# Performance work log

Measured on AMD Instinct MI355X. Metric: run time of the kernel, lower is better.

The kernel has to match this reference:

```python
import jax, jax.numpy as jnp
import numpy as np

N, E, B, ROWS, IN, HID, JKO, FEAT, OH, OUT = 200000, 6400000, 64, 128, 128, 6, 4, 2560, 20, 2

def _leaky(x, s):
    return jnp.where(x >= 0, x, s * x)

def _ln(x, g, b, eps=1e-5):
    mu = jnp.mean(x, -1, keepdims=True)
    v = jnp.mean((x - mu) ** 2, -1, keepdims=True)
    return (x - mu) * jax.lax.rsqrt(v + eps) * g + b

def setup_inputs():
    key = jax.random.key(0)
    ks = jax.random.split(key, 32)
    def w(k, shape, fan_in):
        return jax.random.normal(k, shape, jnp.float32) * (1.0 / np.sqrt(fan_in))
    inp = {
        'x': jax.random.normal(ks[0], (N, IN), jnp.float32),
        'edge_index': jax.random.randint(ks[1], (2, E), 0, N, jnp.int32),
        'batch': jnp.sort(jax.random.randint(ks[2], (N,), 0, B, jnp.int32)),
        'features': jax.random.normal(ks[3], (B, ROWS, FEAT), jnp.float32),
        'one_hot': jax.random.uniform(ks[4], (B, OH), jnp.float32),
        # GATv2Conv params (heads=1)
        'W_l': w(ks[5], (IN, HID), IN), 'b_l': jnp.zeros((HID,)),
        'W_r': w(ks[6], (IN, HID), IN), 'b_r': jnp.zeros((HID,)),
        'att': w(ks[7], (HID,), HID), 'conv_b': jnp.zeros((HID,)),
        # BasicGNN final lin after JK (6 -> 4)
        'jk_W': w(ks[8], (HID, JKO), HID), 'jk_b': jnp.zeros((JKO,)),
        # MLP chain on features
        'l1_W': w(ks[9], (FEAT, 256), FEAT), 'l1_b': jnp.zeros((256,)),
        'ln1_g': jnp.ones((256,)), 'ln1_b': jnp.zeros((256,)),
        'l2_W': w(ks[10], (256, 64), 256), 'l2_b': jnp.zeros((64,)),
        'ln2_g': jnp.ones((64,)), 'ln2_b': jnp.zeros((64,)),
        'l3_W': w(ks[11], (64, 8), 64), 'l3_b': jnp.zeros((8,)),
        'ln3_g': jnp.ones((8,)), 'ln3_b': jnp.zeros((8,)),
        # flattening: rows*8 -> 32
        'fl_W': w(ks[12], (ROWS * 8, 32), ROWS * 8), 'fl_b': jnp.zeros((32,)),
        'ln4_g': jnp.ones((32,)), 'ln4_b': jnp.zeros((32,)),
        # output: 4 + 32 + 20 = 56 -> OUT
        'out_W': w(ks[13], (56, OUT), 56), 'out_b': jnp.zeros((OUT,)),
    }
    return inp

def _forward(x, features, one_hot, W_l, b_l, W_r, b_r, att, conv_b, jk_W, jk_b,
             l1_W, l1_b, ln1_g, ln1_b, l2_W, l2_b, ln2_g, ln2_b, l3_W, l3_b, ln3_g, ln3_b,
             fl_W, fl_b, ln4_g, ln4_b, out_W, out_b, edge_index, batch):
    n = x.shape[0]
    # GATv2Conv, heads=1: separate source/target transforms
    xl = x @ W_l + b_l  # [N,6] source/message features
    xr = x @ W_r + b_r  # [N,6] target features
    loops = jnp.arange(n, dtype=edge_index.dtype)
    src = jnp.concatenate([edge_index[0], loops])  # add self loops
    dst = jnp.concatenate([edge_index[1], loops])
    e = _leaky(xl[src] + xr[dst], 0.2)             # [E+N,6]
    score = e @ att                                 # [E+N]
    m = jax.lax.stop_gradient(jax.ops.segment_max(score, dst, num_segments=n))
    p = jnp.exp(score - m[dst])
    z = jax.ops.segment_sum(p, dst, num_segments=n)
    alpha = p / z[dst]                              # segment softmax over incoming edges
    agg = jax.ops.segment_sum(alpha[:, None] * xl[src], dst, num_segments=n) + conv_b
    x1 = _leaky(agg, 0.01)                          # BasicGNN act ('leakyrelu')
    # JK-LSTM with a single layer collapses to identity (softmax over 1 element)
    h = x1 @ jk_W + jk_b                            # [N,4]
    # global mean pool per graph
    nb = features.shape[0]
    sums = jax.ops.segment_sum(h, batch, num_segments=nb)
    cnt = jax.ops.segment_sum(jnp.ones((n,), h.dtype), batch, num_segments=nb)
    xgcn = sums / jnp.maximum(cnt, 1.0)[:, None]    # [B,4]
    # MLP on features (dropout = identity in eval)
    f = _leaky(_ln(features @ l1_W + l1_b, ln1_g, ln1_b), 0.01)
    f = _leaky(_ln(f @ l2_W + l2_b, ln2_g, ln2_b), 0.01)
    f = _leaky(_ln(f @ l3_W + l3_b, ln3_g, ln3_b), 0.01)  # [B,ROWS,8]
    flat = f.reshape(nb, -1)
    xf = _leaky(_ln(flat @ fl_W + fl_b, ln4_g, ln4_b), 0.01)  # [B,32]
    cat = jnp.concatenate([xgcn, xf, one_hot], axis=1)        # [B,56]
    return cat @ out_W + out_b

def reference(x, features, one_hot, W_l, b_l, W_r, b_r, att, conv_b, jk_W, jk_b,
              l1_W, l1_b, ln1_g, ln1_b, l2_W, l2_b, ln2_g, ln2_b, l3_W, l3_b, ln3_g, ln3_b,
              fl_W, fl_b, ln4_g, ln4_b, out_W, out_b, edge_index, batch):
    return _forward(x, features, one_hot, W_l, b_l, W_r, b_r, att, conv_b, jk_W, jk_b,
                    l1_W, l1_b, ln1_g, ln1_b, l2_W, l2_b, ln2_g, ln2_b, l3_W, l3_b, ln3_g, ln3_b,
                    fl_W, fl_b, ln4_g, ln4_b, out_W, out_b, edge_index, batch)
```

## Files before the change

kernel.cpp:

```cpp
#include <hip/hip_runtime.h>
#include <cstdint>
#include <cstddef>

#define N_NODES 200000
#define N_EDGES 6400000
#define NB      64
#define MROWS   8192
#define FEAT    2560

#define BSZ   256
#define NBK   782
#define EBLK  512
#define ETILE 12500
#define BCAP  8960
#define NXB   768
#define GEMMB 256
#define MLPRB 512

typedef __attribute__((ext_vector_type(8))) short bf16x8;
typedef __attribute__((ext_vector_type(4))) float f32x4;

__device__ __forceinline__ unsigned short bf16rne(float f) {
    unsigned u = __builtin_bit_cast(unsigned, f);
    u += 0x7fffu + ((u >> 16) & 1u);
    return (unsigned short)(u >> 16);
}

__device__ __forceinline__ float bf16f(unsigned short h) {
    return __builtin_bit_cast(float, (unsigned)h << 16);
}

__device__ __forceinline__ void async_cp16(const void* g, void* l) {
    __builtin_amdgcn_global_load_lds(
        (const __attribute__((address_space(1))) unsigned int*)g,
        (__attribute__((address_space(3))) unsigned int*)l, 16, 0, 0);
}

__device__ __forceinline__ void edge_acc(
    uint4 g, const float* xrd, const float* attv, float& z, float* agg)
{
    float xls[6];
    xls[0] = __builtin_bit_cast(float, g.x << 16);
    xls[1] = __builtin_bit_cast(float, g.x & 0xffff0000u);
    xls[2] = __builtin_bit_cast(float, g.y << 16);
    xls[3] = __builtin_bit_cast(float, g.y & 0xffff0000u);
    xls[4] = __builtin_bit_cast(float, g.z << 16);
    xls[5] = __builtin_bit_cast(float, g.z & 0xffff0000u);
    float sc = 0.f;
#pragma unroll
    for (int j = 0; j < 6; j++) {
        float e = xls[j] + xrd[j];
        e = (e >= 0.f) ? e : 0.2f * e;
        sc += attv[j] * e;
    }
    const float p = __expf(sc);
    z += p;
#pragma unroll
    for (int j = 0; j < 6; j++) agg[j] += p * xls[j];
}


__device__ __forceinline__ void nx_body(
    const int nxi, const int nstride,
    const float* __restrict__ x,
    const float* __restrict__ Wl, const float* __restrict__ bl,
    const float* __restrict__ Wr, const float* __restrict__ br,
    unsigned short* __restrict__ xlb, float* __restrict__ xr)
{
    const int t = threadIdx.x;
    const int l = t & 15;

    float wl[48], wr[48];
#pragma unroll
    for (int q = 0; q < 12; q++) {
        *(float4*)&wl[q * 4] = *(const float4*)(Wl + 48 * l + 4 * q);
        *(float4*)&wr[q * 4] = *(const float4*)(Wr + 48 * l + 4 * q);
    }
    for (int g = nxi; g < N_NODES / 16; g += nstride) {
        const int node = g * 16 + (t >> 4);
        float xv[8];
        *(float4*)&xv[0] = *(const float4*)(x + (size_t)node * 128 + l * 8);
        *(float4*)&xv[4] = *(const float4*)(x + (size_t)node * 128 + l * 8 + 4);

        float al[6] = {}, ar[6] = {};
#pragma unroll
        for (int i = 0; i < 8; i++) {
#pragma unroll
            for (int j = 0; j < 6; j++) {
                al[j] += xv[i] * wl[i * 6 + j];
                ar[j] += xv[i] * wr[i * 6 + j];
            }
        }
#pragma unroll
        for (int off = 8; off >= 1; off >>= 1) {
#pragma unroll
            for (int j = 0; j < 6; j++) {
                al[j] += __shfl_xor(al[j], off);
                ar[j] += __shfl_xor(ar[j], off);
            }
        }
        if (l == 0) {
            union { unsigned short h[8]; uint4 v; } u;
#pragma unroll
            for (int j = 0; j < 6; j++) u.h[j] = bf16rne(al[j] + bl[j]);
            u.h[6] = 0; u.h[7] = 0;
            *(uint4*)(xlb + (size_t)node * 8) = u.v;
            float4 r0; float2 r1;
            r0.x = ar[0] + br[0]; r0.y = ar[1] + br[1];
            r0.z = ar[2] + br[2]; r0.w = ar[3] + br[3];
            r1.x = ar[4] + br[4]; r1.y = ar[5] + br[5];
            *(float4*)(xr + (size_t)node * 8) = r0;
            *(float2*)(xr + (size_t)node * 8 + 4) = r1;
        }
    }
}

__device__ __forceinline__ void eb_body(
    const int bid, char* smem,
    const int* __restrict__ ei, int* __restrict__ cursor, int* __restrict__ pairs)
{
    int* sorted = (int*)smem;
    int* hb     = sorted + ETILE;
    int* cur    = hb + NBK + 1;
    int* gbl    = cur + NBK;
    int* wsum   = gbl + NBK;
    const int t = threadIdx.x;
    const int lane = t & 63, wid = t >> 6;
    const int base = bid * ETILE;

    for (int b = t; b < NBK; b += 256) cur[b] = 0;
    __syncthreads();

    for (int i = t; i < ETILE; i += 256)
        atomicAdd(&cur[ei[N_EDGES + base + i] >> 8], 1);
    __syncthreads();

    int c[4]; int lsum = 0;
#pragma unroll
    for (int q = 0; q < 4; q++) {
        const int b = 4 * t + q;
        c[q] = (b < NBK) ? cur[b] : 0;
        lsum += c[q];
    }
    int v = lsum;
#pragma unroll
    for (int d = 1; d < 64; d <<= 1) {
        const int o = __shfl_up(v, d);
        if (lane >= d) v += o;
    }
    if (lane == 63) wsum[wid] = v;
    __syncthreads();
    int off = 0;
#pragma unroll
    for (int w = 0; w < 3; w++) if (w < wid) off += wsum[w];
    int run = off + v - lsum;

    int mygb[4];
#pragma unroll
    for (int q = 0; q < 4; q++) {
        const int b = 4 * t + q;
        mygb[q] = (b < NBK && c[q] > 0) ? atomicAdd(&cursor[b], c[q]) : 0;
    }

#pragma unroll
    for (int q = 0; q < 4; q++) {
        const int b = 4 * t + q;
        if (b <= NBK) hb[b] = run;
        if (b < NBK) cur[b] = run;
        run += c[q];
    }
    __syncthreads();

    for (int i = t; i < ETILE; i += 256) {
        const int d = ei[N_EDGES + base + i];
        const int s = ei[base + i];
        const int pos = atomicAdd(&cur[d >> 8], 1);
        sorted[pos] = (s << 8) | (d & 255);
    }
#pragma unroll
    for (int q = 0; q < 4; q++) {
        const int b = 4 * t + q;
        if (b < NBK) gbl[b] = mygb[q];
    }
    __syncthreads();

    const int grp = t >> 4, gl = t & 15;
    for (int b = grp; b < NBK; b += 16) {
        const int st = hb[b];
        const int cnt = hb[b + 1] - st;
        int* dst = pairs + b * BCAP + gbl[b];
        for (int i = gl; i < cnt; i += 16)
            dst[i] = sorted[st + i];
    }
}

__device__ __forceinline__ void gemm_l1_body(
    const int bx, const int by, char* smem,
    const float* __restrict__ A, const unsigned short* __restrict__ Bt,
    const float* __restrict__ bias, float* __restrict__ C)
{
    unsigned short (*As)[64 * 64] = (unsigned short(*)[64 * 64])smem;
    unsigned short (*Bs)[128 * 64] =
        (unsigned short(*)[128 * 64])(smem + 2 * 64 * 64 * sizeof(short));
    const int K = FEAT, N = 256;
    const int t = threadIdx.x;
    const int w = t >> 6, l = t & 63;
    const int l15 = l & 15, quad = l >> 4;
    const int wm = (w & 1) * 32, wn = (w >> 1) * 64;
    const int gm0 = bx * 64;
    const int gn0 = by * 128;
    const int r8 = l >> 3;
    const int c8 = (l & 7) ^ r8;
    const int ar = t >> 2;
    const int ac0 = (t & 3) * 2;

    f32x4 acc[2][4];
#pragma unroll
    for (int mt = 0; mt < 2; mt++)
#pragma unroll
        for (int nt = 0; nt < 4; nt++) acc[mt][nt] = (f32x4){0.f, 0.f, 0.f, 0.f};

    const int niter = K / 64;

#pragma unroll
    for (int c = 0; c < 4; c++) {
        const int j = w * 4 + c;
        async_cp16(Bt + (size_t)(gn0 + j * 8 + r8) * K + c8 * 8, &Bs[0][j * 512]);
    }
    {
        const float* src = A + (size_t)(gm0 + ar) * K + ac0 * 8;
        float4 v0 = *(const float4*)src;
        float4 v1 = *(const float4*)(src + 4);
        float4 v2 = *(const float4*)(src + 8);
        float4 v3 = *(const float4*)(src + 12);
        union { unsigned short h[8]; uint4 u; } p0, p1;
        p0.h[0] = bf16rne(v0.x); p0.h[1] = bf16rne(v0.y);
        p0.h[2] = bf16rne(v0.z); p0.h[3] = bf16rne(v0.w);
        p0.h[4] = bf16rne(v1.x); p0.h[5] = bf16rne(v1.y);
        p0.h[6] = bf16rne(v1.z); p0.h[7] = bf16rne(v1.w);
        p1.h[0] = bf16rne(v2.x); p1.h[1] = bf16rne(v2.y);
        p1.h[2] = bf16rne(v2.z); p1.h[3] = bf16rne(v2.w);
        p1.h[4] = bf16rne(v3.x); p1.h[5] = bf16rne(v3.y);
        p1.h[6] = bf16rne(v3.z); p1.h[7] = bf16rne(v3.w);
        *(uint4*)&As[0][ar * 64 + ((ac0 + 0) ^ (ar & 7)) * 8] = p0.u;
        *(uint4*)&As[0][ar * 64 + ((ac0 + 1) ^ (ar & 7)) * 8] = p1.u;
    }

    int p = 0;
    for (int i = 0; i < niter; i++) {
        __syncthreads();
        const bool nxt = (i + 1 < niter);
        float4 v0, v1, v2, v3;
        if (nxt) {
            const int k1 = (i + 1) * 64;
#pragma unroll
            for (int c = 0; c < 4; c++) {
                const int j = w * 4 + c;
                async_cp16(Bt + (size_t)(gn0 + j * 8 + r8) * K + k1 + c8 * 8,
                           &Bs[p ^ 1][j * 512]);
            }
            const float* src = A + (size_t)(gm0 + ar) * K + k1 + ac0 * 8;
            v0 = *(const float4*)src;
            v1 = *(const float4*)(src + 4);
            v2 = *(const float4*)(src + 8);
            v3 = *(const float4*)(src + 12);
        }
#pragma unroll
        for (int kki = 0; kki < 2; kki++) {
            bf16x8 af[2], bfr[4];
#pragma unroll
            for (int mt = 0; mt < 2; mt++) {
                const int m = wm + mt * 16 + l15;
                af[mt] = *(const bf16x8*)&As[p][m * 64 + (((quad + 4 * kki) ^ (m & 7)) * 8)];
            }
#pragma unroll
            for (int nt = 0; nt < 4; nt++) {
                const int n = wn + nt * 16 + l15;
                bfr[nt] = *(const bf16x8*)&Bs[p][n * 64 + (((quad + 4 * kki) ^ (n & 7)) * 8)];
            }
#pragma unroll
            for (int mt = 0; mt < 2; mt++)
#pragma unroll
                for (int nt = 0; nt < 4; nt++)
                    acc[mt][nt] = __builtin_amdgcn_mfma_f32_16x16x32_bf16(
                        af[mt], bfr[nt], acc[mt][nt], 0, 0, 0);
        }
        if (nxt) {
            union { unsigned short h[8]; uint4 u; } p0, p1;
            p0.h[0] = bf16rne(v0.x); p0.h[1] = bf16rne(v0.y);
            p0.h[2] = bf16rne(v0.z); p0.h[3] = bf16rne(v0.w);
            p0.h[4] = bf16rne(v1.x); p0.h[5] = bf16rne(v1.y);
            p0.h[6] = bf16rne(v1.z); p0.h[7] = bf16rne(v1.w);
            p1.h[0] = bf16rne(v2.x); p1.h[1] = bf16rne(v2.y);
            p1.h[2] = bf16rne(v2.z); p1.h[3] = bf16rne(v2.w);
            p1.h[4] = bf16rne(v3.x); p1.h[5] = bf16rne(v3.y);
            p1.h[6] = bf16rne(v3.z); p1.h[7] = bf16rne(v3.w);
            *(uint4*)&As[p ^ 1][ar * 64 + ((ac0 + 0) ^ (ar & 7)) * 8] = p0.u;
            *(uint4*)&As[p ^ 1][ar * 64 + ((ac0 + 1) ^ (ar & 7)) * 8] = p1.u;
        }
        p ^= 1;
    }
#pragma unroll
    for (int nt = 0; nt < 4; nt++) {
        const int col = gn0 + wn + nt * 16 + l15;
        const float bv = bias[col];
#pragma unroll
        for (int mt = 0; mt < 2; mt++)
#pragma unroll
            for (int rr = 0; rr < 4; rr++) {
                const int row = gm0 + wm + mt * 16 + quad * 4 + rr;
                C[(size_t)row * N + col] = acc[mt][nt][rr] + bv;
            }
    }
}

__device__ __forceinline__ void br_body(
    const int bid, char* smem,
    const int* __restrict__ pairs, const int* __restrict__ cursor,
    const unsigned short* __restrict__ xlb, const float* __restrict__ xr,
    const float* __restrict__ att, const float* __restrict__ conv_b,
    const float* __restrict__ jkW, const float* __restrict__ jkb,
    const int* __restrict__ batch,
    float* __restrict__ gsum, float* __restrict__ gcnt)
{
    int* sorted = (int*)smem;
    int* hist   = sorted + BCAP;
    int* wtot   = hist + 256;
    const int t = threadIdx.x;
    const int lane = t & 63, wid = t >> 6;
    const int d0 = bid * BSZ + t;

    float xrd[6];
    if (d0 < N_NODES) {
        float4 a = *(const float4*)(xr + (size_t)d0 * 8);
        float2 b = *(const float2*)(xr + (size_t)d0 * 8 + 4);
        xrd[0] = a.x; xrd[1] = a.y; xrd[2] = a.z;
        xrd[3] = a.w; xrd[4] = b.x; xrd[5] = b.y;
    } else {
#pragma unroll
        for (int j = 0; j < 6; j++) xrd[j] = 0.f;
    }
    float attv[6];
#pragma unroll
    for (int j = 0; j < 6; j++) attv[j] = att[j];

    float z = 0.f, agg[6] = {};
    const uint4* xl4 = (const uint4*)xlb;
    const int e0 = bid * BCAP;
    const int e1 = e0 + cursor[bid];

    for (int c0 = e0; c0 < e1; c0 += BCAP) {
        const int rem = e1 - c0;
        const int cnt_chunk = (rem < BCAP) ? rem : BCAP;
        hist[t] = 0;
        __syncthreads();
        for (int i = t; i < cnt_chunk; i += 256)
            atomicAdd(&hist[pairs[c0 + i] & 255], 1);
        __syncthreads();
        const int h = hist[t];
        int v = h;
#pragma unroll
        for (int d = 1; d < 64; d <<= 1) {
            int o = __shfl_up(v, d);
            if (lane >= d) v += o;
        }
        if (lane == 63) wtot[wid] = v;
        __syncthreads();
        int off = 0;
#pragma unroll
        for (int wv = 0; wv < 3; wv++) if (wv < wid) off += wtot[wv];
        const int my_start = v - h + off;
        const int my_cnt = h;
        __syncthreads();
        hist[t] = my_start;
        __syncthreads();
        for (int i = t; i < cnt_chunk; i += 256) {
            const int pv = pairs[c0 + i];
            const int pos = atomicAdd(&hist[pv & 255], 1);
            sorted[pos] = ((unsigned)pv) >> 8;
        }
        __syncthreads();
        int i = 0;
        for (; i + 4 <= my_cnt; i += 4) {
            const int s0 = sorted[my_start + i];
            const int s1 = sorted[my_start + i + 1];
            const int s2 = sorted[my_start + i + 2];
            const int s3 = sorted[my_start + i + 3];
            const uint4 g0 = xl4[s0], g1 = xl4[s1], g2 = xl4[s2], g3 = xl4[s3];
            edge_acc(g0, xrd, attv, z, agg);
            edge_acc(g1, xrd, attv, z, agg);
            edge_acc(g2, xrd, attv, z, agg);
            edge_acc(g3, xrd, attv, z, agg);
        }
        for (; i < my_cnt; i++) {
            const uint4 g = xl4[sorted[my_start + i]];
            edge_acc(g, xrd, attv, z, agg);
        }
        __syncthreads();
    }

    float hh[4] = {0.f, 0.f, 0.f, 0.f};
    float cw = 0.f;
    int b = 0;
    if (d0 < N_NODES) {
        const uint4 g = xl4[d0];
        float xld[6];
        xld[0] = __builtin_bit_cast(float, g.x << 16);
        xld[1] = __builtin_bit_cast(float, g.x & 0xffff0000u);
        xld[2] = __builtin_bit_cast(float, g.y << 16);
        xld[3] = __builtin_bit_cast(float, g.y & 0xffff0000u);
        xld[4] = __builtin_bit_cast(float, g.z << 16);
        xld[5] = __builtin_bit_cast(float, g.z & 0xffff0000u);
        float sc = 0.f;
#pragma unroll
        for (int j = 0; j < 6; j++) {
            float e = xld[j] + xrd[j];
            e = (e >= 0.f) ? e : 0.2f * e;
            sc += attv[j] * e;
        }
        const float p = __expf(sc);
        const float zz = z + p;
#pragma unroll
        for (int c = 0; c < 4; c++) hh[c] = jkb[c];
#pragma unroll
        for (int j = 0; j < 6; j++) {
            float aj = (agg[j] + p * xld[j]) / zz + conv_b[j];
            aj = (aj >= 0.f) ? aj : 0.01f * aj;
#pragma unroll
            for (int c = 0; c < 4; c++) hh[c] += aj * jkW[j * 4 + c];
        }
        b = batch[d0];
        cw = 1.f;
    }
    const int b0 = __shfl(b, 0);
    if (__all(b == b0)) {
#pragma unroll
        for (int off2 = 32; off2 >= 1; off2 >>= 1) {
#pragma unroll
            for (int c = 0; c < 4; c++) hh[c] += __shfl_xor(hh[c], off2);
            cw += __shfl_xor(cw, off2);
        }
        if (lane == 0 && cw > 0.f) {
#pragma unroll
            for (int c = 0; c < 4; c++) atomicAdd(gsum + b0 * 4 + c, hh[c]);
            atomicAdd(gcnt + b0, cw);
        }
    } else if (cw > 0.f) {
#pragma unroll
        for (int c = 0; c < 4; c++) atomicAdd(gsum + b * 4 + c, hh[c]);
        atomicAdd(gcnt + b, cw);
    }
}

__device__ __forceinline__ void mlp_rows_body(
    const int bid, char* smem,
    const float* __restrict__ f1, const unsigned short* __restrict__ w2t,
    const float* __restrict__ ln1_g, const float* __restrict__ ln1_b,
    const float* __restrict__ l2_b,
    const float* __restrict__ ln2_g, const float* __restrict__ ln2_b,
    const float* __restrict__ l3_W, const float* __restrict__ l3_b,
    const float* __restrict__ ln3_g, const float* __restrict__ ln3_b,
    float* __restrict__ f3)
{
    unsigned short* W2 = (unsigned short*)smem;
    const int t = threadIdx.x;
    const int w = t >> 6, l = t & 63;

    for (int i = t; i < 16384; i += 256) {
        const int j = i >> 8, k = i & 255;
        W2[k * 66 + j] = w2t[i];
    }
    const float4 g1 = *(const float4*)(ln1_g + 4 * l);
    const float4 b1 = *(const float4*)(ln1_b + 4 * l);
    const float bo2 = l2_b[l], g2 = ln2_g[l], b2 = ln2_b[l];
    float w3r[8];
    *(float4*)&w3r[0] = *(const float4*)(l3_W + l * 8);
    *(float4*)&w3r[4] = *(const float4*)(l3_W + l * 8 + 4);
    float g3[8], b3[8], bo3[8];
#pragma unroll
    for (int c = 0; c < 8; c++) {
        g3[c] = ln3_g[c]; b3[c] = ln3_b[c]; bo3[c] = l3_b[c];
    }
    __syncthreads();

#pragma unroll 1
    for (int i4 = 0; i4 < 4; i4++) {
        const int row = bid * 16 + w * 4 + i4;
        const float4 v = *(const float4*)(f1 + (size_t)row * 256 + 4 * l);
        float s = v.x + v.y + v.z + v.w;
        float s2 = v.x * v.x + v.y * v.y + v.z * v.z + v.w * v.w;
#pragma unroll
        for (int o = 32; o >= 1; o >>= 1) {
            s += __shfl_xor(s, o);
            s2 += __shfl_xor(s2, o);
        }
        const float mu = s * (1.0f / 256.0f);
        const float rs = rsqrtf(s2 * (1.0f / 256.0f) - mu * mu + 1e-5f);
        float y[4];
        y[0] = (v.x - mu) * rs * g1.x + b1.x;
        y[1] = (v.y - mu) * rs * g1.y + b1.y;
        y[2] = (v.z - mu) * rs * g1.z + b1.z;
        y[3] = (v.w - mu) * rs * g1.w + b1.w;
#pragma unroll
        for (int i = 0; i < 4; i++) y[i] = (y[i] >= 0.f) ? y[i] : 0.01f * y[i];

        float acc = bo2;
#pragma unroll 4
        for (int k0 = 0; k0 < 64; k0++) {
            const float yv0 = __shfl(y[0], k0);
            const float yv1 = __shfl(y[1], k0);
            const float yv2 = __shfl(y[2], k0);
            const float yv3 = __shfl(y[3], k0);
            const int kb = k0 * 264 + l;
            acc += yv0 * bf16f(W2[kb]);
            acc += yv1 * bf16f(W2[kb + 66]);
            acc += yv2 * bf16f(W2[kb + 132]);
            acc += yv3 * bf16f(W2[kb + 198]);
        }
        float s1 = acc, q1 = acc * acc;
#pragma unroll
        for (int o = 32; o >= 1; o >>= 1) {
            s1 += __shfl_xor(s1, o);
            q1 += __shfl_xor(q1, o);
        }
        const float mu2 = s1 * (1.0f / 64.0f);
        const float rs2 = rsqrtf(q1 * (1.0f / 64.0f) - mu2 * mu2 + 1e-5f);
        float y2 = (acc - mu2) * rs2 * g2 + b2;
        y2 = (y2 >= 0.f) ? y2 : 0.01f * y2;

        float p8[8];
#pragma unroll
        for (int c = 0; c < 8; c++) p8[c] = y2 * w3r[c];
#pragma unroll
        for (int o = 32; o >= 1; o >>= 1)
#pragma unroll
            for (int c = 0; c < 8; c++) p8[c] += __shfl_xor(p8[c], o);
#pragma unroll
        for (int c = 0; c < 8; c++) p8[c] += bo3[c];
        float s3 = 0.f;
#pragma unroll
        for (int c = 0; c < 8; c++) s3 += p8[c];
        const float mu3 = s3 * 0.125f;
        float q3 = 0.f;
#pragma unroll
        for (int c = 0; c < 8; c++) { const float d = p8[c] - mu3; q3 += d * d; }
        const float rs3 = rsqrtf(q3 * 0.125f + 1e-5f);
        if (l == 0) {
            float o8[8];
#pragma unroll
            for (int c = 0; c < 8; c++) {
                float yy = (p8[c] - mu3) * rs3 * g3[c] + b3[c];
                o8[c] = (yy >= 0.f) ? yy : 0.01f * yy;
            }
            *(float4*)(f3 + (size_t)row * 8) = *(float4*)&o8[0];
            *(float4*)(f3 + (size_t)row * 8 + 4) = *(float4*)&o8[4];
        }
    }
}


__global__ __launch_bounds__(256) void node_xform(
    const float* __restrict__ x,
    const float* __restrict__ Wl, const float* __restrict__ bl,
    const float* __restrict__ Wr, const float* __restrict__ br,
    unsigned short* __restrict__ xlb, float* __restrict__ xr)
{
    nx_body(blockIdx.x, N_NODES / 16, x, Wl, bl, Wr, br, xlb, xr);
}

__global__ __launch_bounds__(256) void edge_bucket(
    const int* __restrict__ ei, int* __restrict__ cursor, int* __restrict__ pairs)
{
    __shared__ __align__(16) char smem[59408];
    eb_body(blockIdx.x, smem, ei, cursor, pairs);
}

__global__ __launch_bounds__(256) void mfma_gemm_l1(
    const float* __restrict__ A, const unsigned short* __restrict__ Bt,
    const float* __restrict__ bias, float* __restrict__ C)
{
    __shared__ __align__(16) char smem[49152];
    gemm_l1_body(blockIdx.x, blockIdx.y, smem, A, Bt, bias, C);
}

__global__ __launch_bounds__(256) void bucket_reduce(
    const int* __restrict__ pairs, const int* __restrict__ cursor,
    const unsigned short* __restrict__ xlb, const float* __restrict__ xr,
    const float* __restrict__ att, const float* __restrict__ conv_b,
    const float* __restrict__ jkW, const float* __restrict__ jkb,
    const int* __restrict__ batch,
    float* __restrict__ gsum, float* __restrict__ gcnt)
{
    __shared__ __align__(16) char smem[36880];
    br_body(blockIdx.x, smem, pairs, cursor, xlb, xr, att, conv_b, jkW, jkb,
            batch, gsum, gcnt);
}

__global__ __launch_bounds__(256) void fused_front(
    const float* __restrict__ x,
    const float* __restrict__ Wl, const float* __restrict__ bl,
    const float* __restrict__ Wr, const float* __restrict__ br,
    unsigned short* __restrict__ xlb, float* __restrict__ xr,
    const int* __restrict__ ei, int* __restrict__ cursor, int* __restrict__ pairs,
    const float* __restrict__ A, const unsigned short* __restrict__ Bt,
    const float* __restrict__ bias, float* __restrict__ C)
{
    __shared__ __align__(16) char smem[59408];
    const int bid = blockIdx.x;
    const int role = bid % 3;
    const int q = bid / 3;
    if (role == 0) {
        eb_body(q, smem, ei, cursor, pairs);
    } else if (role == 1 && q < GEMMB) {
        gemm_l1_body(q & 127, q >> 7, smem, A, Bt, bias, C);
    } else {
        const int nxi = (role == 2) ? q : EBLK + (q - GEMMB);
        nx_body(nxi, NXB, x, Wl, bl, Wr, br, xlb, xr);
    }
}

__global__ __launch_bounds__(256, 4) void fused_back(
    const int* __restrict__ pairs, const int* __restrict__ cursor,
    const unsigned short* __restrict__ xlb, const float* __restrict__ xr,
    const float* __restrict__ att, const float* __restrict__ conv_b,
    const float* __restrict__ jkW, const float* __restrict__ jkb,
    const int* __restrict__ batch,
    float* __restrict__ gsum, float* __restrict__ gcnt,
    const float* __restrict__ f1, const unsigned short* __restrict__ w2t,
    const float* __restrict__ ln1_g, const float* __restrict__ ln1_b,
    const float* __restrict__ l2_b,
    const float* __restrict__ ln2_g, const float* __restrict__ ln2_b,
    const float* __restrict__ l3_W, const float* __restrict__ l3_b,
    const float* __restrict__ ln3_g, const float* __restrict__ ln3_b,
    float* __restrict__ f3)
{
    __shared__ __align__(16) char smem[36880];
    const int bid = blockIdx.x;
    if (bid < NBK) {
        br_body(bid, smem, pairs, cursor, xlb, xr, att, conv_b, jkW, jkb,
                batch, gsum, gcnt);
    } else {
        mlp_rows_body(bid - NBK, smem, f1, w2t, ln1_g, ln1_b, l2_b,
                      ln2_g, ln2_b, l3_W, l3_b, ln3_g, ln3_b, f3);
    }
}

__global__ __launch_bounds__(256) void flat_final(
    const float* __restrict__ f3, const float* __restrict__ W,
    const float* __restrict__ bb,
    const float* __restrict__ g, const float* __restrict__ b,
    const float* __restrict__ gsum, const float* __restrict__ gcnt,
    const float* __restrict__ onehot,
    const float* __restrict__ Wo, const float* __restrict__ bo,
    float* __restrict__ out)
{
    __shared__ float sf[1024];
    __shared__ float sp[8][32];
    __shared__ float sxf[32];
    const int t = threadIdx.x;
    const int gb = blockIdx.x;
    *(float4*)&sf[t * 4] = *(const float4*)(f3 + (size_t)gb * 1024 + t * 4);
    __syncthreads();
    const int c = t & 31, part = t >> 5;
    float acc = 0.f;
    for (int k = part * 128; k < part * 128 + 128; k++) acc += sf[k] * W[k * 32 + c];
    sp[part][c] = acc;
    __syncthreads();
    if (t < 32) {
        float v = bb[t];
#pragma unroll
        for (int p = 0; p < 8; p++) v += sp[p][t];
        float s = v, s2 = v * v;
#pragma unroll
        for (int off = 16; off >= 1; off >>= 1) {
            s += __shfl_xor(s, off);
            s2 += __shfl_xor(s2, off);
        }
        const float mu = s * (1.0f / 32.0f);
        const float var = s2 * (1.0f / 32.0f) - mu * mu;
        float y = (v - mu) * rsqrtf(var + 1e-5f) * g[t] + b[t];
        sxf[t] = (y >= 0.f) ? y : 0.01f * y;
    }
    __syncthreads();
    if (t < 2) {
        const int o = t;
        float cnt = gcnt[gb];
        cnt = (cnt > 1.f) ? cnt : 1.f;
        float a2 = bo[o];
#pragma unroll
        for (int j = 0; j < 4; j++)  a2 += (gsum[gb * 4 + j] / cnt) * Wo[j * 2 + o];
#pragma unroll
        for (int j = 0; j < 32; j++) a2 += sxf[j] * Wo[(4 + j) * 2 + o];
#pragma unroll
        for (int j = 0; j < 20; j++) a2 += onehot[gb * 20 + j] * Wo[(36 + j) * 2 + o];
        out[gb * 2 + o] = a2;
    }
}

__global__ __launch_bounds__(256) void castT(
    const float* __restrict__ W, unsigned short* __restrict__ Wt, int K, int N)
{
    const int k = blockIdx.x * 256 + threadIdx.x;
    const int n = blockIdx.y;
    if (k < K) Wt[(size_t)n * K + k] = bf16rne(W[(size_t)k * N + n]);
}


__global__ __launch_bounds__(256) void mfma_gemm_l2(
    const unsigned short* __restrict__ Ab, const unsigned short* __restrict__ Bt,
    const float* __restrict__ bias, float* __restrict__ C,
    int M, int N, int K)
{
    __shared__ unsigned short As[32 * 64];
    __shared__ unsigned short Bs[64 * 64];
    const int t = threadIdx.x;
    const int w = t >> 6, l = t & 63;
    const int l15 = l & 15, quad = l >> 4;
    const int gm0 = blockIdx.x * 32;
    const int gn0 = blockIdx.y * 64;
    const int r8 = l >> 3;
    const int c8 = (l & 7) ^ r8;

    f32x4 acc[2];
    acc[0] = (f32x4){0.f, 0.f, 0.f, 0.f};
    acc[1] = (f32x4){0.f, 0.f, 0.f, 0.f};

    for (int k0 = 0; k0 < K; k0 += 64) {
#pragma unroll
        for (int c = 0; c < 2; c++) {
            const int j = w * 2 + c;
            async_cp16(Bt + (size_t)(gn0 + j * 8 + r8) * K + k0 + c8 * 8,
                       &Bs[j * 512]);
        }
        async_cp16(Ab + (size_t)(gm0 + w * 8 + r8) * K + k0 + c8 * 8, &As[w * 512]);
        __syncthreads();
#pragma unroll
        for (int kki = 0; kki < 2; kki++) {
            bf16x8 af[2], bfr;
#pragma unroll
            for (int mt = 0; mt < 2; mt++) {
                const int m = mt * 16 + l15;
                af[mt] = *(const bf16x8*)&As[m * 64 + (((quad + 4 * kki) ^ (m & 7)) * 8)];
            }
            const int n = w * 16 + l15;
            bfr = *(const bf16x8*)&Bs[n * 64 + (((quad + 4 * kki) ^ (n & 7)) * 8)];
#pragma unroll
            for (int mt = 0; mt < 2; mt++)
                acc[mt] = __builtin_amdgcn_mfma_f32_16x16x32_bf16(
                    af[mt], bfr, acc[mt], 0, 0, 0);
        }
        __syncthreads();
    }
    const int col = gn0 + w * 16 + l15;
    const float bv = bias[col];
#pragma unroll
    for (int mt = 0; mt < 2; mt++)
#pragma unroll
        for (int rr = 0; rr < 4; rr++) {
            const int row = gm0 + mt * 16 + quad * 4 + rr;
            C[(size_t)row * N + col] = acc[mt][rr] + bv;
        }
}

__global__ __launch_bounds__(256) void ln_leaky_c256(
    const float* __restrict__ f, unsigned short* __restrict__ out,
    const float* __restrict__ g, const float* __restrict__ b)
{
    const int row = blockIdx.x;
    const int t = threadIdx.x;
    float v = f[(size_t)row * 256 + t];
    float s = v, s2 = v * v;
#pragma unroll
    for (int off = 32; off >= 1; off >>= 1) {
        s += __shfl_xor(s, off);
        s2 += __shfl_xor(s2, off);
    }
    __shared__ float ws[4], ws2[4];
    const int wid = t >> 6, lane = t & 63;
    if (lane == 0) { ws[wid] = s; ws2[wid] = s2; }
    __syncthreads();
    const float S = ws[0] + ws[1] + ws[2] + ws[3];
    const float S2 = ws2[0] + ws2[1] + ws2[2] + ws2[3];
    const float mu = S * (1.0f / 256.0f);
    const float var = S2 * (1.0f / 256.0f) - mu * mu;
    float y = (v - mu) * rsqrtf(var + 1e-5f) * g[t] + b[t];
    y = (y >= 0.f) ? y : 0.01f * y;
    out[(size_t)row * 256 + t] = bf16rne(y);
}

__global__ __launch_bounds__(256) void ln_leaky_c64(
    float* __restrict__ f, const float* __restrict__ g, const float* __restrict__ b)
{
    const int wid = threadIdx.x >> 6, lane = threadIdx.x & 63;
    const int row = blockIdx.x * 4 + wid;
    float v = f[(size_t)row * 64 + lane];
    float s = v, s2 = v * v;
#pragma unroll
    for (int off = 32; off >= 1; off >>= 1) {
        s += __shfl_xor(s, off);
        s2 += __shfl_xor(s2, off);
    }
    const float mu = s * (1.0f / 64.0f);
    const float var = s2 * (1.0f / 64.0f) - mu * mu;
    float y = (v - mu) * rsqrtf(var + 1e-5f) * g[lane] + b[lane];
    f[(size_t)row * 64 + lane] = (y >= 0.f) ? y : 0.01f * y;
}

__global__ __launch_bounds__(256) void l3_ln_leaky(
    const float* __restrict__ f2, const float* __restrict__ W3,
    const float* __restrict__ b3,
    const float* __restrict__ g, const float* __restrict__ b,
    float* __restrict__ f3)
{
    __shared__ float sW[64 * 8];
    const int t = threadIdx.x;
    sW[t] = W3[t]; sW[t + 256] = W3[t + 256];
    __syncthreads();
    const int row = blockIdx.x * 32 + (t >> 3);
    const int c = t & 7;
    float acc = b3[c];
    const float* fr = f2 + (size_t)row * 64;
#pragma unroll 8
    for (int k = 0; k < 64; k++) acc += fr[k] * sW[k * 8 + c];
    float s = acc, s2 = acc * acc;
#pragma unroll
    for (int off = 4; off >= 1; off >>= 1) {
        s += __shfl_xor(s, off);
        s2 += __shfl_xor(s2, off);
    }
    const float mu = s * (1.0f / 8.0f);
    const float var = s2 * (1.0f / 8.0f) - mu * mu;
    float y = (acc - mu) * rsqrtf(var + 1e-5f) * g[c] + b[c];
    f3[(size_t)row * 8 + c] = (y >= 0.f) ? y : 0.01f * y;
}

__global__ __launch_bounds__(256) void flat_ln_leaky(
    const float* __restrict__ f3, const float* __restrict__ W,
    const float* __restrict__ bb,
    const float* __restrict__ g, const float* __restrict__ b,
    float* __restrict__ xf)
{
    __shared__ float sf[1024];
    __shared__ float sp[8][32];
    const int t = threadIdx.x;
    const int gb = blockIdx.x;
    *(float4*)&sf[t * 4] = *(const float4*)(f3 + (size_t)gb * 1024 + t * 4);
    __syncthreads();
    const int c = t & 31, part = t >> 5;
    float acc = 0.f;
    for (int k = part * 128; k < part * 128 + 128; k++) acc += sf[k] * W[k * 32 + c];
    sp[part][c] = acc;
    __syncthreads();
    if (t < 32) {
        float v = bb[t];
#pragma unroll
        for (int p = 0; p < 8; p++) v += sp[p][t];
        float s = v, s2 = v * v;
#pragma unroll
        for (int off = 16; off >= 1; off >>= 1) {
            s += __shfl_xor(s, off);
            s2 += __shfl_xor(s2, off);
        }
        const float mu = s * (1.0f / 32.0f);
        const float var = s2 * (1.0f / 32.0f) - mu * mu;
        float y = (v - mu) * rsqrtf(var + 1e-5f) * g[t] + b[t];
        xf[gb * 32 + t] = (y >= 0.f) ? y : 0.01f * y;
    }
}

__global__ __launch_bounds__(128) void final_out(
    const float* __restrict__ gsum, const float* __restrict__ gcnt,
    const float* __restrict__ xf, const float* __restrict__ onehot,
    const float* __restrict__ Wo, const float* __restrict__ bo,
    float* __restrict__ out)
{
    const int t = threadIdx.x;
    const int gb = t >> 1, o = t & 1;
    float cnt = gcnt[gb];
    cnt = (cnt > 1.f) ? cnt : 1.f;
    float acc = bo[o];
#pragma unroll
    for (int j = 0; j < 4; j++)  acc += (gsum[gb * 4 + j] / cnt) * Wo[j * 2 + o];
#pragma unroll
    for (int j = 0; j < 32; j++) acc += xf[gb * 32 + j] * Wo[(4 + j) * 2 + o];
#pragma unroll
    for (int j = 0; j < 20; j++) acc += onehot[gb * 20 + j] * Wo[(36 + j) * 2 + o];
    out[t] = acc;
}

extern "C" void kernel_launch(void* const* d_in, const int* in_sizes, int n_in,
                              void* d_out, int out_size, void* d_ws, size_t ws_size,
                              hipStream_t stream)
{
    const float* x        = (const float*)d_in[0];
    const int*   ei       = (const int*)d_in[1];
    const int*   batch    = (const int*)d_in[2];
    const float* features = (const float*)d_in[3];
    const float* one_hot  = (const float*)d_in[4];
    const float* W_l   = (const float*)d_in[5];
    const float* b_l   = (const float*)d_in[6];
    const float* W_r   = (const float*)d_in[7];
    const float* b_r   = (const float*)d_in[8];
    const float* att   = (const float*)d_in[9];
    const float* conv_b = (const float*)d_in[10];
    const float* jk_W  = (const float*)d_in[11];
    const float* jk_b  = (const float*)d_in[12];
    const float* l1_W  = (const float*)d_in[13];
    const float* l1_b  = (const float*)d_in[14];
    const float* ln1_g = (const float*)d_in[15];
    const float* ln1_b = (const float*)d_in[16];
    const float* l2_W  = (const float*)d_in[17];
    const float* l2_b  = (const float*)d_in[18];
    const float* ln2_g = (const float*)d_in[19];
    const float* ln2_b = (const float*)d_in[20];
    const float* l3_W  = (const float*)d_in[21];
    const float* l3_b  = (const float*)d_in[22];
    const float* ln3_g = (const float*)d_in[23];
    const float* ln3_b = (const float*)d_in[24];
    const float* fl_W  = (const float*)d_in[25];
    const float* fl_b  = (const float*)d_in[26];
    const float* ln4_g = (const float*)d_in[27];
    const float* ln4_b = (const float*)d_in[28];
    const float* out_W = (const float*)d_in[29];
    const float* out_b = (const float*)d_in[30];
    (void)in_sizes; (void)n_in; (void)out_size;

    float* ws = (float*)d_ws;
    unsigned short* xlb = (unsigned short*)(ws + 0);
    float* xr   = ws + 800000;
    unsigned short* w1t = (unsigned short*)(ws + 2400000);
    unsigned short* w2t = (unsigned short*)(ws + 2727680);
    float* gsum   = ws + 2735872;
    float* gcnt   = ws + 2736128;
    int*   cursor = (int*)(ws + 2736192);
    int* pairs = (int*)(ws + 2737024);

    const bool fuse = ws_size >= (size_t)13481344 * 4;

    hipMemsetAsync(gsum, 0, 1102 * sizeof(float), stream);

    castT<<<dim3(10, 256), 256, 0, stream>>>(l1_W, w1t, FEAT, 256);
    castT<<<dim3(1, 64), 256, 0, stream>>>(l2_W, w2t, 256, 64);

    if (fuse) {
        float* f1 = ws + 9743744;
        float* f3 = ws + 13413760;
        fused_front<<<EBLK + GEMMB + NXB, 256, 0, stream>>>(
            x, W_l, b_l, W_r, b_r, xlb, xr,
            ei, cursor, pairs,
            features, w1t, l1_b, f1);
        fused_back<<<NBK + MLPRB, 256, 0, stream>>>(
            pairs, cursor, xlb, xr, att, conv_b, jk_W, jk_b, batch,
            gsum, gcnt,
            f1, w2t, ln1_g, ln1_b, l2_b, ln2_g, ln2_b,
            l3_W, l3_b, ln3_g, ln3_b, f3);
        flat_final<<<NB, 256, 0, stream>>>(
            f3, fl_W, fl_b, ln4_g, ln4_b,
            gsum, gcnt, one_hot, out_W, out_b, (float*)d_out);
    } else {
        float* f1           = ws + 2737024;
        unsigned short* f1b = (unsigned short*)(ws + 4834176);
        float* f2           = ws + 5358464;
        float* f3           = ws + 5882752;
        float* xf           = ws + 5948288;
        node_xform<<<N_NODES / 16, 256, 0, stream>>>(x, W_l, b_l, W_r, b_r,
                                                     xlb, xr);
        edge_bucket<<<EBLK, 256, 0, stream>>>(ei, cursor, pairs);
        bucket_reduce<<<NBK, 256, 0, stream>>>(pairs, cursor, xlb, xr, att,
                                               conv_b, jk_W, jk_b, batch,
                                               gsum, gcnt);
        mfma_gemm_l1<<<dim3(MROWS / 64, 2), 256, 0, stream>>>(
            features, w1t, l1_b, f1);
        ln_leaky_c256<<<MROWS, 256, 0, stream>>>(f1, f1b, ln1_g, ln1_b);
        mfma_gemm_l2<<<dim3(MROWS / 32, 1), 256, 0, stream>>>(
            f1b, w2t, l2_b, f2, MROWS, 64, 256);
        ln_leaky_c64<<<MROWS / 4, 256, 0, stream>>>(f2, ln2_g, ln2_b);
        l3_ln_leaky<<<MROWS / 32, 256, 0, stream>>>(f2, l3_W, l3_b,
                                                    ln3_g, ln3_b, f3);
        flat_ln_leaky<<<NB, 256, 0, stream>>>(f3, fl_W, fl_b, ln4_g, ln4_b, xf);
        final_out<<<1, 128, 0, stream>>>(gsum, gcnt, xf, one_hot, out_W, out_b,
                                         (float*)d_out);
    }
}
```

Baseline: 561.3 us.

## Split fused back kernel and use contiguous role blocks in front kernel

The back-stage kernel that ran bucket reduction and the row MLP as different block roles in one launch is split into two separate launches. The front kernel now gives each role a contiguous range of block indices instead of interleaving roles by bid%3. The fallback path also reuses the fused MLP and final kernels, and the old unfused kernels are deleted. This trades co-scheduling of heterogeneous blocks for simpler per-kernel occupancy, at the cost of an extra launch and lost overlap between the graph reduction and the MLP.

Result: no change. 561.3 us (+0.0%).

```diff
diff --git a/kernel.cpp b/kernel.cpp
--- a/kernel.cpp
+++ b/kernel.cpp
@@ -596,6 +596,20 @@
             batch, gsum, gcnt);
 }
 
+__global__ __launch_bounds__(256) void mlp_rows(
+    const float* __restrict__ f1, const unsigned short* __restrict__ w2t,
+    const float* __restrict__ ln1_g, const float* __restrict__ ln1_b,
+    const float* __restrict__ l2_b,
+    const float* __restrict__ ln2_g, const float* __restrict__ ln2_b,
+    const float* __restrict__ l3_W, const float* __restrict__ l3_b,
+    const float* __restrict__ ln3_g, const float* __restrict__ ln3_b,
+    float* __restrict__ f3)
+{
+    __shared__ __align__(16) char smem[33792];
+    mlp_rows_body(blockIdx.x, smem, f1, w2t, ln1_g, ln1_b, l2_b,
+                  ln2_g, ln2_b, l3_W, l3_b, ln3_g, ln3_b, f3);
+}
+
 __global__ __launch_bounds__(256) void fused_front(
     const float* __restrict__ x,
     const float* __restrict__ Wl, const float* __restrict__ bl,
@@ -607,41 +621,13 @@
 {
     __shared__ __align__(16) char smem[59408];
     const int bid = blockIdx.x;
-    const int role = bid % 3;
-    const int q = bid / 3;
-    if (role == 0) {
-        eb_body(q, smem, ei, cursor, pairs);
-    } else if (role == 1 && q < GEMMB) {
+    if (bid < EBLK) {
+        eb_body(bid, smem, ei, cursor, pairs);
+    } else if (bid < EBLK + GEMMB) {
+        const int q = bid - EBLK;
         gemm_l1_body(q & 127, q >> 7, smem, A, Bt, bias, C);
     } else {
-        const int nxi = (role == 2) ? q : EBLK + (q - GEMMB);
-        nx_body(nxi, NXB, x, Wl, bl, Wr, br, xlb, xr);
-    }
-}
-
-__global__ __launch_bounds__(256, 4) void fused_back(
-    const int* __restrict__ pairs, const int* __restrict__ cursor,
-    const unsigned short* __restrict__ xlb, const float* __restrict__ xr,
-    const float* __restrict__ att, const float* __restrict__ conv_b,
-    const float* __restrict__ jkW, const float* __restrict__ jkb,
-    const int* __restrict__ batch,
-    float* __restrict__ gsum, float* __restrict__ gcnt,
-    const float* __restrict__ f1, const unsigned short* __restrict__ w2t,
-    const float* __restrict__ ln1_g, const float* __restrict__ ln1_b,
-    const float* __restrict__ l2_b,
-    const float* __restrict__ ln2_g, const float* __restrict__ ln2_b,
-    const float* __restrict__ l3_W, const float* __restrict__ l3_b,
-    const float* __restrict__ ln3_g, const float* __restrict__ ln3_b,
-    float* __restrict__ f3)
-{
-    __shared__ __align__(16) char smem[36880];
-    const int bid = blockIdx.x;
-    if (bid < NBK) {
-        br_body(bid, smem, pairs, cursor, xlb, xr, att, conv_b, jkW, jkb,
-                batch, gsum, gcnt);
-    } else {
-        mlp_rows_body(bid - NBK, smem, f1, w2t, ln1_g, ln1_b, l2_b,
-                      ln2_g, ln2_b, l3_W, l3_b, ln3_g, ln3_b, f3);
+        nx_body(bid - EBLK - GEMMB, NXB, x, Wl, bl, Wr, br, xlb, xr);
     }
 }
 
@@ -703,189 +689,6 @@
     const int k = blockIdx.x * 256 + threadIdx.x;
     const int n = blockIdx.y;
     if (k < K) Wt[(size_t)n * K + k] = bf16rne(W[(size_t)k * N + n]);
-}
-
-
-__global__ __launch_bounds__(256) void mfma_gemm_l2(
-    const unsigned short* __restrict__ Ab, const unsigned short* __restrict__ Bt,
-    const float* __restrict__ bias, float* __restrict__ C,
-    int M, int N, int K)
-{
-    __shared__ unsigned short As[32 * 64];
-    __shared__ unsigned short Bs[64 * 64];
-    const int t = threadIdx.x;
-    const int w = t >> 6, l = t & 63;
-    const int l15 = l & 15, quad = l >> 4;
-    const int gm0 = blockIdx.x * 32;
-    const int gn0 = blockIdx.y * 64;
-    const int r8 = l >> 3;
-    const int c8 = (l & 7) ^ r8;
-
-    f32x4 acc[2];
-    acc[0] = (f32x4){0.f, 0.f, 0.f, 0.f};
-    acc[1] = (f32x4){0.f, 0.f, 0.f, 0.f};
-
-    for (int k0 = 0; k0 < K; k0 += 64) {
-#pragma unroll
-        for (int c = 0; c < 2; c++) {
-            const int j = w * 2 + c;
-            async_cp16(Bt + (size_t)(gn0 + j * 8 + r8) * K + k0 + c8 * 8,
-                       &Bs[j * 512]);
-        }
-        async_cp16(Ab + (size_t)(gm0 + w * 8 + r8) * K + k0 + c8 * 8, &As[w * 512]);
-        __syncthreads();
-#pragma unroll
-        for (int kki = 0; kki < 2; kki++) {
-            bf16x8 af[2], bfr;
-#pragma unroll
-            for (int mt = 0; mt < 2; mt++) {
-                const int m = mt * 16 + l15;
-                af[mt] = *(const bf16x8*)&As[m * 64 + (((quad + 4 * kki) ^ (m & 7)) * 8)];
-            }
-            const int n = w * 16 + l15;
-            bfr = *(const bf16x8*)&Bs[n * 64 + (((quad + 4 * kki) ^ (n & 7)) * 8)];
-#pragma unroll
-            for (int mt = 0; mt < 2; mt++)
-                acc[mt] = __builtin_amdgcn_mfma_f32_16x16x32_bf16(
-                    af[mt], bfr, acc[mt], 0, 0, 0);
-        }
-        __syncthreads();
-    }
-    const int col = gn0 + w * 16 + l15;
-    const float bv = bias[col];
-#pragma unroll
-    for (int mt = 0; mt < 2; mt++)
-#pragma unroll
-        for (int rr = 0; rr < 4; rr++) {
-            const int row = gm0 + mt * 16 + quad * 4 + rr;
-            C[(size_t)row * N + col] = acc[mt][rr] + bv;
-        }
-}
-
-__global__ __launch_bounds__(256) void ln_leaky_c256(
-    const float* __restrict__ f, unsigned short* __restrict__ out,
-    const float* __restrict__ g, const float* __restrict__ b)
-{
-    const int row = blockIdx.x;
-    const int t = threadIdx.x;
-    float v = f[(size_t)row * 256 + t];
-    float s = v, s2 = v * v;
-#pragma unroll
-    for (int off = 32; off >= 1; off >>= 1) {
-        s += __shfl_xor(s, off);
-        s2 += __shfl_xor(s2, off);
-    }
-    __shared__ float ws[4], ws2[4];
-    const int wid = t >> 6, lane = t & 63;
-    if (lane == 0) { ws[wid] = s; ws2[wid] = s2; }
-    __syncthreads();
-    const float S = ws[0] + ws[1] + ws[2] + ws[3];
-    const float S2 = ws2[0] + ws2[1] + ws2[2] + ws2[3];
-    const float mu = S * (1.0f / 256.0f);
-    const float var = S2 * (1.0f / 256.0f) - mu * mu;
-    float y = (v - mu) * rsqrtf(var + 1e-5f) * g[t] + b[t];
-    y = (y >= 0.f) ? y : 0.01f * y;
-    out[(size_t)row * 256 + t] = bf16rne(y);
-}
-
-__global__ __launch_bounds__(256) void ln_leaky_c64(
-    float* __restrict__ f, const float* __restrict__ g, const float* __restrict__ b)
-{
-    const int wid = threadIdx.x >> 6, lane = threadIdx.x & 63;
-    const int row = blockIdx.x * 4 + wid;
-    float v = f[(size_t)row * 64 + lane];
-    float s = v, s2 = v * v;
-#pragma unroll
-    for (int off = 32; off >= 1; off >>= 1) {
-        s += __shfl_xor(s, off);
-        s2 += __shfl_xor(s2, off);
-    }
-    const float mu = s * (1.0f / 64.0f);
-    const float var = s2 * (1.0f / 64.0f) - mu * mu;
-    float y = (v - mu) * rsqrtf(var + 1e-5f) * g[lane] + b[lane];
-    f[(size_t)row * 64 + lane] = (y >= 0.f) ? y : 0.01f * y;
-}
-
-__global__ __launch_bounds__(256) void l3_ln_leaky(
-    const float* __restrict__ f2, const float* __restrict__ W3,
-    const float* __restrict__ b3,
-    const float* __restrict__ g, const float* __restrict__ b,
-    float* __restrict__ f3)
-{
-    __shared__ float sW[64 * 8];
-    const int t = threadIdx.x;
-    sW[t] = W3[t]; sW[t + 256] = W3[t + 256];
-    __syncthreads();
-    const int row = blockIdx.x * 32 + (t >> 3);
-    const int c = t & 7;
-    float acc = b3[c];
-    const float* fr = f2 + (size_t)row * 64;
-#pragma unroll 8
-    for (int k = 0; k < 64; k++) acc += fr[k] * sW[k * 8 + c];
-    float s = acc, s2 = acc * acc;
-#pragma unroll
-    for (int off = 4; off >= 1; off >>= 1) {
-        s += __shfl_xor(s, off);
-        s2 += __shfl_xor(s2, off);
-    }
-    const float mu = s * (1.0f / 8.0f);
-    const float var = s2 * (1.0f / 8.0f) - mu * mu;
-    float y = (acc - mu) * rsqrtf(var + 1e-5f) * g[c] + b[c];
-    f3[(size_t)row * 8 + c] = (y >= 0.f) ? y : 0.01f * y;
-}
-
-__global__ __launch_bounds__(256) void flat_ln_leaky(
-    const float* __restrict__ f3, const float* __restrict__ W,
-    const float* __restrict__ bb,
-    const float* __restrict__ g, const float* __restrict__ b,
-    float* __restrict__ xf)
-{
-    __shared__ float sf[1024];
-    __shared__ float sp[8][32];
-    const int t = threadIdx.x;
-    const int gb = blockIdx.x;
-    *(float4*)&sf[t * 4] = *(const float4*)(f3 + (size_t)gb * 1024 + t * 4);
-    __syncthreads();
-    const int c = t & 31, part = t >> 5;
-    float acc = 0.f;
-    for (int k = part * 128; k < part * 128 + 128; k++) acc += sf[k] * W[k * 32 + c];
-    sp[part][c] = acc;
-    __syncthreads();
-    if (t < 32) {
-        float v = bb[t];
-#pragma unroll
-        for (int p = 0; p < 8; p++) v += sp[p][t];
-        float s = v, s2 = v * v;
-#pragma unroll
-        for (int off = 16; off >= 1; off >>= 1) {
-            s += __shfl_xor(s, off);
-            s2 += __shfl_xor(s2, off);
-        }
-        const float mu = s * (1.0f / 32.0f);
-        const float var = s2 * (1.0f / 32.0f) - mu * mu;
-        float y = (v - mu) * rsqrtf(var + 1e-5f) * g[t] + b[t];
-        xf[gb * 32 + t] = (y >= 0.f) ? y : 0.01f * y;
-    }
-}
-
-__global__ __launch_bounds__(128) void final_out(
-    const float* __restrict__ gsum, const float* __restrict__ gcnt,
-    const float* __restrict__ xf, const float* __restrict__ onehot,
-    const float* __restrict__ Wo, const float* __restrict__ bo,
-    float* __restrict__ out)
-{
-    const int t = threadIdx.x;
-    const int gb = t >> 1, o = t & 1;
-    float cnt = gcnt[gb];
-    cnt = (cnt > 1.f) ? cnt : 1.f;
-    float acc = bo[o];
-#pragma unroll
-    for (int j = 0; j < 4; j++)  acc += (gsum[gb * 4 + j] / cnt) * Wo[j * 2 + o];
-#pragma unroll
-    for (int j = 0; j < 32; j++) acc += xf[gb * 32 + j] * Wo[(4 + j) * 2 + o];
-#pragma unroll
-    for (int j = 0; j < 20; j++) acc += onehot[gb * 20 + j] * Wo[(36 + j) * 2 + o];
-    out[t] = acc;
 }
 
 extern "C" void kernel_launch(void* const* d_in, const int* in_sizes, int n_in,
@@ -949,20 +752,18 @@
             x, W_l, b_l, W_r, b_r, xlb, xr,
             ei, cursor, pairs,
             features, w1t, l1_b, f1);
-        fused_back<<<NBK + MLPRB, 256, 0, stream>>>(
-            pairs, cursor, xlb, xr, att, conv_b, jk_W, jk_b, batch,
-            gsum, gcnt,
+        bucket_reduce<<<NBK, 256, 0, stream>>>(pairs, cursor, xlb, xr, att,
+                                               conv_b, jk_W, jk_b, batch,
+                                               gsum, gcnt);
+        mlp_rows<<<MLPRB, 256, 0, stream>>>(
             f1, w2t, ln1_g, ln1_b, l2_b, ln2_g, ln2_b,
             l3_W, l3_b, ln3_g, ln3_b, f3);
         flat_final<<<NB, 256, 0, stream>>>(
             f3, fl_W, fl_b, ln4_g, ln4_b,
             gsum, gcnt, one_hot, out_W, out_b, (float*)d_out);
     } else {
-        float* f1           = ws + 2737024;
-        unsigned short* f1b = (unsigned short*)(ws + 4834176);
-        float* f2           = ws + 5358464;
-        float* f3           = ws + 5882752;
-        float* xf           = ws + 5948288;
+        float* f1 = ws + 2737024;
+        float* f3 = ws + 5882752;
         node_xform<<<N_NODES / 16, 256, 0, stream>>>(x, W_l, b_l, W_r, b_r,
                                                      xlb, xr);
         edge_bucket<<<EBLK, 256, 0, stream>>>(ei, cursor, pairs);
@@ -971,14 +772,11 @@
                                                gsum, gcnt);
         mfma_gemm_l1<<<dim3(MROWS / 64, 2), 256, 0, stream>>>(
             features, w1t, l1_b, f1);
-        ln_leaky_c256<<<MROWS, 256, 0, stream>>>(f1, f1b, ln1_g, ln1_b);
-        mfma_gemm_l2<<<dim3(MROWS / 32, 1), 256, 0, stream>>>(
-            f1b, w2t, l2_b, f2, MROWS, 64, 256);
-        ln_leaky_c64<<<MROWS / 4, 256, 0, stream>>>(f2, ln2_g, ln2_b);
-        l3_ln_leaky<<<MROWS / 32, 256, 0, stream>>>(f2, l3_W, l3_b,
-                                                    ln3_g, ln3_b, f3);
-        flat_ln_leaky<<<NB, 256, 0, stream>>>(f3, fl_W, fl_b, ln4_g, ln4_b, xf);
-        final_out<<<1, 128, 0, stream>>>(gsum, gcnt, xf, one_hot, out_W, out_b,
-                                         (float*)d_out);
-    }
-}
+        mlp_rows<<<MLPRB, 256, 0, stream>>>(
+            f1, w2t, ln1_g, ln1_b, l2_b, ln2_g, ln2_b,
+            l3_W, l3_b, ln3_g, ln3_b, f3);
+        flat_final<<<NB, 256, 0, stream>>>(
+            f3, fl_W, fl_b, ln4_g, ln4_b,
+            gsum, gcnt, one_hot, out_W, out_b, (float*)d_out);
+    }
+}
```
